# Kernel tuning notes

Measured on AMD Instinct MI355X. Metric: run time of the kernel, lower is better.

## Reference

```python
import jax, jax.numpy as jnp
import numpy as np

N = 10000          # total nodes
N_AGENTS = 5000    # drones (x[:, -1] < 0)
E = 160000         # random edges (self-loops added in reference)
C_IN, H, C_HID, C_OUT = 16, 8, 128, 8
NEG_SLOPE = 0.2    # GATv2Conv default leaky_relu slope


def setup_inputs() -> dict:
    key = jax.random.key(0)
    ks = jax.random.split(key, 12)
    x = jax.random.normal(ks[0], (N, C_IN), dtype=jnp.float32)
    # last feature column encodes node type: <0 -> drone, >=0 -> goal
    type_col = jnp.where(jnp.arange(N) < N_AGENTS, -1.0, 1.0).astype(jnp.float32)
    x = x.at[:, -1].set(type_col)
    edge_index = jax.random.randint(ks[1], (2, E), 0, N, dtype=jnp.int32)
    s = 0.1  # glorot-ish scale
    return {
        "x": x,
        "edge_index": edge_index,
        "Wl1": s * jax.random.normal(ks[2], (C_IN, H * C_HID), jnp.float32),
        "bl1": jnp.zeros((H * C_HID,), jnp.float32),
        "Wr1": s * jax.random.normal(ks[3], (C_IN, H * C_HID), jnp.float32),
        "br1": jnp.zeros((H * C_HID,), jnp.float32),
        "att1": s * jax.random.normal(ks[4], (H, C_HID), jnp.float32),
        "b1": jnp.zeros((C_HID,), jnp.float32),
        "Wl2": s * jax.random.normal(ks[5], (C_HID, H * C_HID), jnp.float32),
        "bl2": jnp.zeros((H * C_HID,), jnp.float32),
        "Wr2": s * jax.random.normal(ks[6], (C_HID, H * C_HID), jnp.float32),
        "br2": jnp.zeros((H * C_HID,), jnp.float32),
        "att2": s * jax.random.normal(ks[7], (H, C_HID), jnp.float32),
        "b2": jnp.zeros((C_HID,), jnp.float32),
        "Wlin": s * jax.random.normal(ks[8], (C_HID, C_OUT), jnp.float32),
        "blin": jnp.zeros((C_OUT,), jnp.float32),
    }


def gatv2_conv(x, src, dst, Wl, bl, Wr, br, att, bias):
    """PyG GATv2Conv, heads=H, concat=False (head-mean), add_self_loops handled by caller."""
    n = x.shape[0]
    xl = (x @ Wl + bl).reshape(n, H, -1)   # [N,H,C] source transform
    xr = (x @ Wr + br).reshape(n, H, -1)   # [N,H,C] target transform
    e = jax.nn.leaky_relu(xl[src] + xr[dst], NEG_SLOPE)          # [E,H,C]
    alpha = jnp.einsum("ehc,hc->eh", e, att)                      # [E,H]
    # per-destination softmax over incoming edges
    m = jax.ops.segment_max(alpha, dst, num_segments=n)
    a = jnp.exp(alpha - m[dst])
    denom = jax.ops.segment_sum(a, dst, num_segments=n)
    a = a / (denom[dst] + 1e-16)
    out = jax.ops.segment_sum(xl[src] * a[:, :, None], dst, num_segments=n)  # [N,H,C]
    return out.mean(axis=1) + bias  # concat=False -> mean over heads


def reference(x, edge_index, Wl1, bl1, Wr1, br1, att1, b1,
              Wl2, bl2, Wr2, br2, att2, b2, Wlin, blin):
    n = x.shape[0]
    loops = jnp.arange(n, dtype=edge_index.dtype)
    src = jnp.concatenate([edge_index[0], loops])
    dst = jnp.concatenate([edge_index[1], loops])
    drone_mask = x[:, -1] < 0
    y = x  # bounds is None -> no division
    h = jax.nn.relu(gatv2_conv(y, src, dst, Wl1, bl1, Wr1, br1, att1, b1))
    h = jax.nn.relu(gatv2_conv(h, src, dst, Wl2, bl2, Wr2, br2, att2, b2))
    out = h @ Wlin + blin  # [N, C_OUT]
    idx = jnp.nonzero(drone_mask, size=N_AGENTS)[0]
    return out[idx]  # [N_AGENTS, C_OUT]
```

## Files before the change

kernel.cpp:

```cpp
#include <hip/hip_runtime.h>
#include <hip/hip_fp16.h>
#include <math.h>

#define N_NODES 10000
#define N_EDGES 160000
#define NAG     5000
#define HC      1024
#define CH      128
#define NEG     0.2f
#define BCAP    64

#define NSCAT   625
#define NGEMM   1256

typedef _Float16 f16x8 __attribute__((ext_vector_type(8)));
typedef _Float16 f16x2 __attribute__((ext_vector_type(2)));
typedef float f32x4 __attribute__((ext_vector_type(4)));

__device__ __forceinline__ __half2 pk_max(__half2 a, __half2 b) {
    __half2 r;
    asm volatile("v_pk_max_f16 %0, %1, %2" : "=v"(r) : "v"(a), "v"(b));
    return r;
}

__device__ __forceinline__ void edge_accum(float4 raw, const __half2* xr2, const __half2* att2,
                                           float& lsum, float* acc, bool valid) {
    __half2* hp = (__half2*)&raw;
    const __half2 neg2 = __float2half2_rn(NEG);
    float p = 0.f;
    #pragma unroll
    for (int j = 0; j < 4; j++) {
        __half2 z = __hadd2(hp[j], xr2[j]);
        __half2 lz = pk_max(z, __hmul2(z, neg2));
#if __has_builtin(__builtin_amdgcn_fdot2)
        p = __builtin_amdgcn_fdot2(*(f16x2*)&lz, *(const f16x2*)&att2[j], p, false);
#else
        float2 lf = __half22float2(lz);
        float2 af = __half22float2(att2[j]);
        p = fmaf(lf.x, af.x, p);
        p = fmaf(lf.y, af.y, p);
#endif
    }
    p += __shfl_xor(p, 1, 64);
    p += __shfl_xor(p, 2, 64);
    p += __shfl_xor(p, 4, 64);
    p += __shfl_xor(p, 8, 64);
    float w = valid ? __expf(p) : 0.f;
    lsum += w;
    #pragma unroll
    for (int j = 0; j < 4; j++) {
        acc[2 * j]     = fmaf(__low2float(hp[j]),  w, acc[2 * j]);
        acc[2 * j + 1] = fmaf(__high2float(hp[j]), w, acc[2 * j + 1]);
    }
}

template <int K, int KA>
__device__ void gemm_tile(char* smem, int vt,
                          const float* __restrict__ A,
                          const _Float16* __restrict__ Whl, const float* __restrict__ bl,
                          const _Float16* __restrict__ Whr, const float* __restrict__ br,
                          _Float16* __restrict__ xl, float* __restrict__ xr,
                          int limitL, int limitR) {
    _Float16* ash = (_Float16*)smem;
    float (*eps)[68] = (float(*)[68])smem;
    const int AS = K + 8;
    int by = vt & 7;
    int rowblk = (vt >> 3) * 64;
    bool right = by >= 4;
    if (rowblk >= (right ? limitR : limitL)) return;
    const _Float16* Wh = right ? Whr : Whl;
    const float* bs    = right ? br : bl;
    int colbase = (by & 3) * 256;
    int t = threadIdx.x;
    int w = t >> 6, l = t & 63;
    int m = l & 15, q = l >> 4;

    for (int idx = t; idx < 64 * (K / 8); idx += 256) {
        int r  = idx / (K / 8);
        int c8 = (idx % (K / 8)) * 8;
        int row = rowblk + r;
        float4 v0 = make_float4(0.f, 0.f, 0.f, 0.f);
        float4 v1 = make_float4(0.f, 0.f, 0.f, 0.f);
        if (row < N_NODES && c8 < KA) {
            v0 = *(const float4*)(A + (size_t)row * KA + c8);
            v1 = *(const float4*)(A + (size_t)row * KA + c8 + 4);
        }
        f16x8 hv;
        hv[0] = (_Float16)v0.x; hv[1] = (_Float16)v0.y; hv[2] = (_Float16)v0.z; hv[3] = (_Float16)v0.w;
        hv[4] = (_Float16)v1.x; hv[5] = (_Float16)v1.y; hv[6] = (_Float16)v1.z; hv[7] = (_Float16)v1.w;
        *(f16x8*)&ash[r * AS + c8] = hv;
    }
    __syncthreads();

    f32x4 acc[16];
    #pragma unroll
    for (int i = 0; i < 16; i++) acc[i] = (f32x4){0.f, 0.f, 0.f, 0.f};

    #pragma unroll
    for (int kq = 0; kq < K / 32; kq++) {
        f16x8 af = *(const f16x8*)&ash[(w * 16 + m) * AS + kq * 32 + q * 8];
        const _Float16* base = Wh + (((size_t)(kq * 64 + (colbase >> 4))) << 9) + l * 8;
        #pragma unroll
        for (int tile = 0; tile < 16; tile++) {
            f16x8 bf = *(const f16x8*)(base + ((size_t)tile << 9));
            acc[tile] = __builtin_amdgcn_mfma_f32_16x16x32_f16(af, bf, acc[tile], 0, 0, 0);
        }
    }

    float bv[16];
    #pragma unroll
    for (int tile = 0; tile < 16; tile++) bv[tile] = bs[colbase + tile * 16 + m];

    for (int cgk = 0; cgk < 4; cgk++) {
        __syncthreads();
        #pragma unroll
        for (int tt = 0; tt < 4; tt++) {
            int tile = cgk * 4 + tt;
            int cl = tt * 16 + m;
            #pragma unroll
            for (int reg = 0; reg < 4; reg++)
                eps[w * 16 + q * 4 + reg][cl] = acc[tile][reg] + bv[tile];
        }
        __syncthreads();
        int colg = colbase + cgk * 64;
        int cc = (t & 15) * 4;
        #pragma unroll
        for (int it = 0; it < 4; it++) {
            int r = it * 16 + (t >> 4);
            int row = rowblk + r;
            if (row < N_NODES) {
                float4 v = *(const float4*)&eps[r][cc];
                if (right) {
                    *(float4*)(xr + (size_t)row * HC + colg + cc) = v;
                } else {
                    __half2 h01 = __floats2half2_rn(v.x, v.y);
                    __half2 h23 = __floats2half2_rn(v.z, v.w);
                    float2 st;
                    st.x = *(float*)&h01;
                    st.y = *(float*)&h23;
                    *(float2*)(xl + (size_t)row * HC + colg + cc) = st;
                }
            }
        }
    }
}

template <int LAYER>
__device__ void gat_phase(char* smem, int ndst,
                          const __half* __restrict__ xl, const float* __restrict__ xr,
                          const float* __restrict__ att, const float* __restrict__ bias,
                          const int* __restrict__ cnt, const int* __restrict__ srcs,
                          float* __restrict__ h_out,
                          const float* __restrict__ Wlin, const float* __restrict__ blin,
                          float* __restrict__ out) {
    float* part  = (float*)smem;
    float* lpart = (float*)(smem + 8192);
    float* hrow  = (float*)(smem + 8256);
    int t = threadIdx.x;
    int slot = t >> 7;
    int c0 = (t & 127) * 8;

    for (int dstn = blockIdx.x; dstn < ndst; dstn += gridDim.x) {
        __half2 xr2[4], att2[4];
        {
            float4 a0 = *(const float4*)(xr + (size_t)dstn * HC + c0);
            float4 a1 = *(const float4*)(xr + (size_t)dstn * HC + c0 + 4);
            xr2[0] = __floats2half2_rn(a0.x, a0.y);
            xr2[1] = __floats2half2_rn(a0.z, a0.w);
            xr2[2] = __floats2half2_rn(a1.x, a1.y);
            xr2[3] = __floats2half2_rn(a1.z, a1.w);
            float4 b0 = *(const float4*)(att + c0);
            float4 b1 = *(const float4*)(att + c0 + 4);
            att2[0] = __floats2half2_rn(b0.x, b0.y);
            att2[1] = __floats2half2_rn(b0.z, b0.w);
            att2[2] = __floats2half2_rn(b1.x, b1.y);
            att2[3] = __floats2half2_rn(b1.z, b1.w);
        }

        float acc[8];
        #pragma unroll
        for (int j = 0; j < 8; j++) acc[j] = 0.f;
        float lsum = 0.f;

        int e0 = dstn << 6;
        int e1 = e0 + cnt[dstn];
        int e = e0;
        for (; e + 16 <= e1; e += 16) {
            int s[8];
            #pragma unroll
            for (int i = 0; i < 8; i++) s[i] = srcs[e + slot + 2 * i];
            float4 raw[8];
            #pragma unroll
            for (int i = 0; i < 8; i++) raw[i] = *(const float4*)(xl + (size_t)s[i] * HC + c0);
            #pragma unroll
            for (int i = 0; i < 8; i++) edge_accum(raw[i], xr2, att2, lsum, acc, true);
        }
        for (; e + 4 <= e1; e += 4) {
            int s[2];
            #pragma unroll
            for (int i = 0; i < 2; i++) s[i] = srcs[e + slot + 2 * i];
            float4 raw[2];
            #pragma unroll
            for (int i = 0; i < 2; i++) raw[i] = *(const float4*)(xl + (size_t)s[i] * HC + c0);
            #pragma unroll
            for (int i = 0; i < 2; i++) edge_accum(raw[i], xr2, att2, lsum, acc, true);
        }
        for (; e < e1; e += 2) {
            int ee = e + slot;
            bool valid = ee < e1;
            int s = srcs[valid ? ee : e];
            float4 raw = *(const float4*)(xl + (size_t)s * HC + c0);
            edge_accum(raw, xr2, att2, lsum, acc, valid);
        }

        #pragma unroll
        for (int j = 0; j < 8; j++) part[slot * HC + c0 + j] = acc[j];
        if ((t & 15) == 0) lpart[slot * 8 + (c0 >> 7)] = lsum;
        __syncthreads();

        if (t < 128) {
            int head = t >> 4;
            float lv = lpart[head] + lpart[8 + head];
            float inv = 1.f / (lv + 1e-16f);
            #pragma unroll
            for (int j = 0; j < 8; j++) {
                int c = t * 8 + j;
                part[c] = (part[c] + part[HC + c]) * inv;
            }
        }
        __syncthreads();
        if (t < 128) {
            float ssum = 0.f;
            #pragma unroll
            for (int h = 0; h < 8; h++) ssum += part[h * 128 + t];
            float val = fmaxf(ssum * 0.125f + bias[t], 0.f);
            if (LAYER == 1) h_out[(size_t)dstn * CH + t] = val;
            else hrow[t] = val;
        }
        if (LAYER == 2) {
            __syncthreads();
            if (t < 64) {
                int j = t & 7, p8 = t >> 3;
                float v = 0.f;
                #pragma unroll
                for (int kk = 0; kk < 16; kk++) {
                    int k = p8 * 16 + kk;
                    v = fmaf(hrow[k], Wlin[k * 8 + j], v);
                }
                v += __shfl_xor(v, 8, 64);
                v += __shfl_xor(v, 16, 64);
                v += __shfl_xor(v, 32, 64);
                if (t < 8) out[(size_t)dstn * 8 + t] = v + blin[t];
            }
        }
        __syncthreads();
    }
}

__device__ __forceinline__ void emit_frag(const float* __restrict__ W, _Float16* __restrict__ o,
                                          int gid, int KAreal) {
    int f = gid >> 9, rem = gid & 511;
    int l = rem >> 3, j = rem & 7;
    int kq = f >> 6, tile = f & 63;
    int m = l & 15, q = l >> 4;
    int col = tile * 16 + m;
    int k = kq * 32 + q * 8 + j;
    float v = (k < KAreal) ? W[k * 1024 + col] : 0.f;
    o[gid] = (_Float16)v;
}

__global__ __launch_bounds__(256) void prep_kernel(const float* __restrict__ Wl1, const float* __restrict__ Wr1,
                                                   const float* __restrict__ Wl2, const float* __restrict__ Wr2,
                                                   _Float16* __restrict__ w1l, _Float16* __restrict__ w1r,
                                                   _Float16* __restrict__ w2l, _Float16* __restrict__ w2r,
                                                   int* __restrict__ cnt, int* __restrict__ srcs) {
    int t = threadIdx.x;
    if (blockIdx.x < 40) {
        int i = blockIdx.x * 256 + t;
        if (i < N_NODES) {
            cnt[i] = 1;
            srcs[i << 6] = i;
        }
        return;
    }
    int gid = (blockIdx.x - 40) * 256 + t;
    const int S1 = 1024 * 32, S2 = 1024 * 128;
    if (gid < S1)               emit_frag(Wl1, w1l, gid, 16);
    else if (gid < 2 * S1)      emit_frag(Wr1, w1r, gid - S1, 16);
    else if (gid < 2 * S1 + S2) emit_frag(Wl2, w2l, gid - 2 * S1, 128);
    else if (gid < 2 * (S1 + S2)) emit_frag(Wr2, w2r, gid - 2 * S1 - S2, 128);
}

__global__ __launch_bounds__(256) void scatter_gemm1_kernel(const int* __restrict__ esrc,
                                                            const int* __restrict__ edst,
                                                            int* __restrict__ cnt,
                                                            int* __restrict__ srcs,
                                                            const float* __restrict__ x,
                                                            const _Float16* __restrict__ w1l, const float* __restrict__ bl1,
                                                            const _Float16* __restrict__ w1r, const float* __restrict__ br1,
                                                            _Float16* __restrict__ xlh, float* __restrict__ xr) {
    __shared__ __align__(16) char smem[17408];
    if (blockIdx.x < NSCAT) {
        int e = blockIdx.x * 256 + threadIdx.x;
        int d = edst[e];
        int p = atomicAdd(&cnt[d], 1);
        if (p < BCAP) srcs[(d << 6) + p] = esrc[e];
    } else {
        gemm_tile<32, 16>(smem, blockIdx.x - NSCAT, x, w1l, bl1, w1r, br1,
                          xlh, xr, N_NODES, N_NODES);
    }
}

__global__ __launch_bounds__(256) void gemm2_kernel(const float* __restrict__ h1,
                                                    const _Float16* __restrict__ w2l, const float* __restrict__ bl2,
                                                    const _Float16* __restrict__ w2r, const float* __restrict__ br2,
                                                    _Float16* __restrict__ xlh, float* __restrict__ xr) {
    __shared__ __align__(16) char smem[17408];
    gemm_tile<128, 128>(smem, blockIdx.x, h1, w2l, bl2, w2r, br2, xlh, xr, N_NODES, NAG);
}

template <int LAYER>
__global__ __launch_bounds__(256) void gat_kernel(const __half* __restrict__ xl,
                                                  const float* __restrict__ xr,
                                                  const float* __restrict__ att,
                                                  const float* __restrict__ bias,
                                                  const int* __restrict__ cnt,
                                                  const int* __restrict__ srcs,
                                                  float* __restrict__ h_out,
                                                  const float* __restrict__ Wlin,
                                                  const float* __restrict__ blin,
                                                  float* __restrict__ out,
                                                  int ndst) {
    __shared__ __align__(16) char smem[8768];
    gat_phase<LAYER>(smem, ndst, xl, xr, att, bias, cnt, srcs, h_out, Wlin, blin, out);
}

extern "C" void kernel_launch(void* const* d_in, const int* in_sizes, int n_in,
                              void* d_out, int out_size, void* d_ws, size_t ws_size,
                              hipStream_t stream) {
    const float* x    = (const float*)d_in[0];
    const int*   ei   = (const int*)d_in[1];
    const float* Wl1  = (const float*)d_in[2];
    const float* bl1  = (const float*)d_in[3];
    const float* Wr1  = (const float*)d_in[4];
    const float* br1  = (const float*)d_in[5];
    const float* att1 = (const float*)d_in[6];
    const float* b1   = (const float*)d_in[7];
    const float* Wl2  = (const float*)d_in[8];
    const float* bl2  = (const float*)d_in[9];
    const float* Wr2  = (const float*)d_in[10];
    const float* br2  = (const float*)d_in[11];
    const float* att2 = (const float*)d_in[12];
    const float* b2   = (const float*)d_in[13];
    const float* Wlin = (const float*)d_in[14];
    const float* blin = (const float*)d_in[15];
    float* out = (float*)d_out;

    const int* esrc = ei;
    const int* edst = ei + N_EDGES;

    char* p = (char*)d_ws;
    __half* xlh = (__half*)p;                  p += (size_t)N_NODES * HC * sizeof(__half);
    float*  xr  = (float*)p;                   p += (size_t)N_NODES * HC * sizeof(float);
    float*  h1  = (float*)p;                   p += (size_t)N_NODES * CH * sizeof(float);
    _Float16* w1l = (_Float16*)p;              p += 1024 * 32 * sizeof(_Float16);
    _Float16* w1r = (_Float16*)p;              p += 1024 * 32 * sizeof(_Float16);
    _Float16* w2l = (_Float16*)p;              p += 1024 * 128 * sizeof(_Float16);
    _Float16* w2r = (_Float16*)p;              p += 1024 * 128 * sizeof(_Float16);
    int* cnt  = (int*)p;                       p += (size_t)N_NODES * sizeof(int) + 64;
    int* srcs = (int*)p;

    prep_kernel<<<40 + 1280, 256, 0, stream>>>(Wl1, Wr1, Wl2, Wr2, w1l, w1r, w2l, w2r, cnt, srcs);
    scatter_gemm1_kernel<<<NSCAT + NGEMM, 256, 0, stream>>>(esrc, edst, cnt, srcs, x,
                                                            w1l, bl1, w1r, br1,
                                                            (_Float16*)xlh, xr);
    gat_kernel<1><<<N_NODES, 256, 0, stream>>>(xlh, xr, att1, b1, cnt, srcs,
                                               h1, nullptr, nullptr, nullptr, N_NODES);
    gemm2_kernel<<<NGEMM, 256, 0, stream>>>(h1, w2l, bl2, w2r, br2, (_Float16*)xlh, xr);
    gat_kernel<2><<<NAG, 256, 0, stream>>>(xlh, xr, att2, b2, cnt, srcs,
                                           nullptr, Wlin, blin, out, NAG);
}
```

Measured before the change: 243.1 us.

## Store xr and h1 in fp16 and move layer-2 weight prep into gemm1 kernel

The right-side projection xr and the layer-1 hidden output h1 are now stored in fp16 instead of fp32, which halves the bytes written by both GEMMs and read by the GAT kernels. The layer-2 weight fragment conversion moves out of the prep kernel into the combined gemm1/scatter kernel, so the prep kernel gets shorter and that work overlaps with other blocks. Block order in the fused kernel is reordered to put GEMM tiles first. xr was already rounded to half inside the GAT kernel, so the main accuracy risk comes from rounding h1 to fp16.

```diff
diff --git a/kernel.cpp b/kernel.cpp
--- a/kernel.cpp
+++ b/kernel.cpp
@@ -12,6 +12,7 @@
 
 #define NSCAT   625
 #define NGEMM   1256
+#define NW2     1024
 
 typedef _Float16 f16x8 __attribute__((ext_vector_type(8)));
 typedef _Float16 f16x2 __attribute__((ext_vector_type(2)));
@@ -54,12 +55,12 @@
     }
 }
 
-template <int K, int KA>
+template <int K, int KA, typename AT>
 __device__ void gemm_tile(char* smem, int vt,
-                          const float* __restrict__ A,
+                          const AT* __restrict__ A,
                           const _Float16* __restrict__ Whl, const float* __restrict__ bl,
                           const _Float16* __restrict__ Whr, const float* __restrict__ br,
-                          _Float16* __restrict__ xl, float* __restrict__ xr,
+                          _Float16* __restrict__ xl, _Float16* __restrict__ xr,
                           int limitL, int limitR) {
     _Float16* ash = (_Float16*)smem;
     float (*eps)[68] = (float(*)[68])smem;
@@ -70,6 +71,7 @@
     if (rowblk >= (right ? limitR : limitL)) return;
     const _Float16* Wh = right ? Whr : Whl;
     const float* bs    = right ? br : bl;
+    _Float16* outp     = right ? xr : xl;
     int colbase = (by & 3) * 256;
     int t = threadIdx.x;
     int w = t >> 6, l = t & 63;
@@ -79,15 +81,17 @@
         int r  = idx / (K / 8);
         int c8 = (idx % (K / 8)) * 8;
         int row = rowblk + r;
-        float4 v0 = make_float4(0.f, 0.f, 0.f, 0.f);
-        float4 v1 = make_float4(0.f, 0.f, 0.f, 0.f);
+        f16x8 hv = (f16x8){0, 0, 0, 0, 0, 0, 0, 0};
         if (row < N_NODES && c8 < KA) {
-            v0 = *(const float4*)(A + (size_t)row * KA + c8);
-            v1 = *(const float4*)(A + (size_t)row * KA + c8 + 4);
-        }
-        f16x8 hv;
-        hv[0] = (_Float16)v0.x; hv[1] = (_Float16)v0.y; hv[2] = (_Float16)v0.z; hv[3] = (_Float16)v0.w;
-        hv[4] = (_Float16)v1.x; hv[5] = (_Float16)v1.y; hv[6] = (_Float16)v1.z; hv[7] = (_Float16)v1.w;
+            if constexpr (sizeof(AT) == 2) {
+                hv = *(const f16x8*)((const _Float16*)A + (size_t)row * KA + c8);
+            } else {
+                float4 v0 = *(const float4*)((const float*)A + (size_t)row * KA + c8);
+                float4 v1 = *(const float4*)((const float*)A + (size_t)row * KA + c8 + 4);
+                hv[0] = (_Float16)v0.x; hv[1] = (_Float16)v0.y; hv[2] = (_Float16)v0.z; hv[3] = (_Float16)v0.w;
+                hv[4] = (_Float16)v1.x; hv[5] = (_Float16)v1.y; hv[6] = (_Float16)v1.z; hv[7] = (_Float16)v1.w;
+            }
+        }
         *(f16x8*)&ash[r * AS + c8] = hv;
     }
     __syncthreads();
@@ -130,16 +134,12 @@
             int row = rowblk + r;
             if (row < N_NODES) {
                 float4 v = *(const float4*)&eps[r][cc];
-                if (right) {
-                    *(float4*)(xr + (size_t)row * HC + colg + cc) = v;
-                } else {
-                    __half2 h01 = __floats2half2_rn(v.x, v.y);
-                    __half2 h23 = __floats2half2_rn(v.z, v.w);
-                    float2 st;
-                    st.x = *(float*)&h01;
-                    st.y = *(float*)&h23;
-                    *(float2*)(xl + (size_t)row * HC + colg + cc) = st;
-                }
+                __half2 h01 = __floats2half2_rn(v.x, v.y);
+                __half2 h23 = __floats2half2_rn(v.z, v.w);
+                float2 st;
+                st.x = *(float*)&h01;
+                st.y = *(float*)&h23;
+                *(float2*)(outp + (size_t)row * HC + colg + cc) = st;
             }
         }
     }
@@ -147,10 +147,10 @@
 
 template <int LAYER>
 __device__ void gat_phase(char* smem, int ndst,
-                          const __half* __restrict__ xl, const float* __restrict__ xr,
+                          const __half* __restrict__ xl, const _Float16* __restrict__ xr,
                           const float* __restrict__ att, const float* __restrict__ bias,
                           const int* __restrict__ cnt, const int* __restrict__ srcs,
-                          float* __restrict__ h_out,
+                          _Float16* __restrict__ h_out,
                           const float* __restrict__ Wlin, const float* __restrict__ blin,
                           float* __restrict__ out) {
     float* part  = (float*)smem;
@@ -163,12 +163,9 @@
     for (int dstn = blockIdx.x; dstn < ndst; dstn += gridDim.x) {
         __half2 xr2[4], att2[4];
         {
-            float4 a0 = *(const float4*)(xr + (size_t)dstn * HC + c0);
-            float4 a1 = *(const float4*)(xr + (size_t)dstn * HC + c0 + 4);
-            xr2[0] = __floats2half2_rn(a0.x, a0.y);
-            xr2[1] = __floats2half2_rn(a0.z, a0.w);
-            xr2[2] = __floats2half2_rn(a1.x, a1.y);
-            xr2[3] = __floats2half2_rn(a1.z, a1.w);
+            f16x8 xv = *(const f16x8*)(xr + (size_t)dstn * HC + c0);
+            __half2* xp = (__half2*)&xv;
+            xr2[0] = xp[0]; xr2[1] = xp[1]; xr2[2] = xp[2]; xr2[3] = xp[3];
             float4 b0 = *(const float4*)(att + c0);
             float4 b1 = *(const float4*)(att + c0 + 4);
             att2[0] = __floats2half2_rn(b0.x, b0.y);
@@ -234,7 +231,7 @@
             #pragma unroll
             for (int h = 0; h < 8; h++) ssum += part[h * 128 + t];
             float val = fmaxf(ssum * 0.125f + bias[t], 0.f);
-            if (LAYER == 1) h_out[(size_t)dstn * CH + t] = val;
+            if (LAYER == 1) h_out[(size_t)dstn * CH + t] = (_Float16)val;
             else hrow[t] = val;
         }
         if (LAYER == 2) {
@@ -270,9 +267,7 @@
 }
 
 __global__ __launch_bounds__(256) void prep_kernel(const float* __restrict__ Wl1, const float* __restrict__ Wr1,
-                                                   const float* __restrict__ Wl2, const float* __restrict__ Wr2,
                                                    _Float16* __restrict__ w1l, _Float16* __restrict__ w1r,
-                                                   _Float16* __restrict__ w2l, _Float16* __restrict__ w2r,
                                                    int* __restrict__ cnt, int* __restrict__ srcs) {
     int t = threadIdx.x;
     if (blockIdx.x < 40) {
@@ -284,49 +279,56 @@
         return;
     }
     int gid = (blockIdx.x - 40) * 256 + t;
-    const int S1 = 1024 * 32, S2 = 1024 * 128;
-    if (gid < S1)               emit_frag(Wl1, w1l, gid, 16);
-    else if (gid < 2 * S1)      emit_frag(Wr1, w1r, gid - S1, 16);
-    else if (gid < 2 * S1 + S2) emit_frag(Wl2, w2l, gid - 2 * S1, 128);
-    else if (gid < 2 * (S1 + S2)) emit_frag(Wr2, w2r, gid - 2 * S1 - S2, 128);
-}
-
-__global__ __launch_bounds__(256) void scatter_gemm1_kernel(const int* __restrict__ esrc,
-                                                            const int* __restrict__ edst,
-                                                            int* __restrict__ cnt,
-                                                            int* __restrict__ srcs,
-                                                            const float* __restrict__ x,
-                                                            const _Float16* __restrict__ w1l, const float* __restrict__ bl1,
-                                                            const _Float16* __restrict__ w1r, const float* __restrict__ br1,
-                                                            _Float16* __restrict__ xlh, float* __restrict__ xr) {
+    const int S1 = 1024 * 32;
+    if (gid < S1)          emit_frag(Wl1, w1l, gid, 16);
+    else if (gid < 2 * S1) emit_frag(Wr1, w1r, gid - S1, 16);
+}
+
+__global__ __launch_bounds__(256) void d2_kernel(const int* __restrict__ esrc,
+                                                 const int* __restrict__ edst,
+                                                 int* __restrict__ cnt,
+                                                 int* __restrict__ srcs,
+                                                 const float* __restrict__ x,
+                                                 const _Float16* __restrict__ w1l, const float* __restrict__ bl1,
+                                                 const _Float16* __restrict__ w1r, const float* __restrict__ br1,
+                                                 _Float16* __restrict__ xlh, _Float16* __restrict__ xrh,
+                                                 const float* __restrict__ Wl2, const float* __restrict__ Wr2,
+                                                 _Float16* __restrict__ w2l, _Float16* __restrict__ w2r) {
     __shared__ __align__(16) char smem[17408];
-    if (blockIdx.x < NSCAT) {
-        int e = blockIdx.x * 256 + threadIdx.x;
+    int b = blockIdx.x;
+    if (b < NGEMM) {
+        gemm_tile<32, 16, float>(smem, b, x, w1l, bl1, w1r, br1,
+                                 xlh, xrh, N_NODES, N_NODES);
+    } else if (b < NGEMM + NSCAT) {
+        int e = (b - NGEMM) * 256 + threadIdx.x;
         int d = edst[e];
         int p = atomicAdd(&cnt[d], 1);
         if (p < BCAP) srcs[(d << 6) + p] = esrc[e];
     } else {
-        gemm_tile<32, 16>(smem, blockIdx.x - NSCAT, x, w1l, bl1, w1r, br1,
-                          xlh, xr, N_NODES, N_NODES);
-    }
-}
-
-__global__ __launch_bounds__(256) void gemm2_kernel(const float* __restrict__ h1,
+        int gid = (b - NGEMM - NSCAT) * 256 + threadIdx.x;
+        const int S2 = 1024 * 128;
+        if (gid < S2)          emit_frag(Wl2, w2l, gid, 128);
+        else if (gid < 2 * S2) emit_frag(Wr2, w2r, gid - S2, 128);
+    }
+}
+
+__global__ __launch_bounds__(256) void gemm2_kernel(const _Float16* __restrict__ h1,
                                                     const _Float16* __restrict__ w2l, const float* __restrict__ bl2,
                                                     const _Float16* __restrict__ w2r, const float* __restrict__ br2,
-                                                    _Float16* __restrict__ xlh, float* __restrict__ xr) {
+                                                    _Float16* __restrict__ xlh, _Float16* __restrict__ xrh) {
     __shared__ __align__(16) char smem[17408];
-    gemm_tile<128, 128>(smem, blockIdx.x, h1, w2l, bl2, w2r, br2, xlh, xr, N_NODES, NAG);
+    gemm_tile<128, 128, _Float16>(smem, blockIdx.x, h1, w2l, bl2, w2r, br2,
+                                  xlh, xrh, N_NODES, NAG);
 }
 
 template <int LAYER>
 __global__ __launch_bounds__(256) void gat_kernel(const __half* __restrict__ xl,
-                                                  const float* __restrict__ xr,
+                                                  const _Float16* __restrict__ xr,
                                                   const float* __restrict__ att,
                                                   const float* __restrict__ bias,
                                                   const int* __restrict__ cnt,
                                                   const int* __restrict__ srcs,
-                                                  float* __restrict__ h_out,
+                                                  _Float16* __restrict__ h_out,
                                                   const float* __restrict__ Wlin,
                                                   const float* __restrict__ blin,
                                                   float* __restrict__ out,
@@ -360,9 +362,9 @@
     const int* edst = ei + N_EDGES;
 
     char* p = (char*)d_ws;
-    __half* xlh = (__half*)p;                  p += (size_t)N_NODES * HC * sizeof(__half);
-    float*  xr  = (float*)p;                   p += (size_t)N_NODES * HC * sizeof(float);
-    float*  h1  = (float*)p;                   p += (size_t)N_NODES * CH * sizeof(float);
+    __half* xlh    = (__half*)p;               p += (size_t)N_NODES * HC * sizeof(__half);
+    _Float16* xrh  = (_Float16*)p;             p += (size_t)N_NODES * HC * sizeof(_Float16);
+    _Float16* h1   = (_Float16*)p;             p += (size_t)N_NODES * CH * sizeof(_Float16);
     _Float16* w1l = (_Float16*)p;              p += 1024 * 32 * sizeof(_Float16);
     _Float16* w1r = (_Float16*)p;              p += 1024 * 32 * sizeof(_Float16);
     _Float16* w2l = (_Float16*)p;              p += 1024 * 128 * sizeof(_Float16);
@@ -370,13 +372,14 @@
     int* cnt  = (int*)p;                       p += (size_t)N_NODES * sizeof(int) + 64;
     int* srcs = (int*)p;
 
-    prep_kernel<<<40 + 1280, 256, 0, stream>>>(Wl1, Wr1, Wl2, Wr2, w1l, w1r, w2l, w2r, cnt, srcs);
-    scatter_gemm1_kernel<<<NSCAT + NGEMM, 256, 0, stream>>>(esrc, edst, cnt, srcs, x,
-                                                            w1l, bl1, w1r, br1,
-                                                            (_Float16*)xlh, xr);
-    gat_kernel<1><<<N_NODES, 256, 0, stream>>>(xlh, xr, att1, b1, cnt, srcs,
+    prep_kernel<<<40 + 256, 256, 0, stream>>>(Wl1, Wr1, w1l, w1r, cnt, srcs);
+    d2_kernel<<<NGEMM + NSCAT + NW2, 256, 0, stream>>>(esrc, edst, cnt, srcs, x,
+                                                       w1l, bl1, w1r, br1,
+                                                       (_Float16*)xlh, xrh,
+                                                       Wl2, Wr2, w2l, w2r);
+    gat_kernel<1><<<N_NODES, 256, 0, stream>>>(xlh, xrh, att1, b1, cnt, srcs,
                                                h1, nullptr, nullptr, nullptr, N_NODES);
-    gemm2_kernel<<<NGEMM, 256, 0, stream>>>(h1, w2l, bl2, w2r, br2, (_Float16*)xlh, xr);
-    gat_kernel<2><<<NAG, 256, 0, stream>>>(xlh, xr, att2, b2, cnt, srcs,
+    gemm2_kernel<<<NGEMM, 256, 0, stream>>>(h1, w2l, bl2, w2r, br2, (_Float16*)xlh, xrh);
+    gat_kernel<2><<<NAG, 256, 0, stream>>>(xlh, xrh, att2, b2, cnt, srcs,
                                            nullptr, Wlin, blin, out, NAG);
 }
```

New measurement: 243.0 us. About the same (-0.0%).
